# Kernel tuning notes

Hardware: AMD Instinct MI355X
Metric: run time of the kernel (lower is better)

The kernel has to match this reference:

```python
import jax, jax.numpy as jnp
import numpy as np

N, IN_DIM, INTER, HID, OUT, G = 8192, 512, 512, 1024, 512, 16
EPS = 1e-5


def setup_inputs() -> dict:
    key = jax.random.key(0)
    ks = jax.random.split(key, 16)
    s = 0.02
    return {
        "h": jax.random.normal(ks[0], (N, IN_DIM), jnp.float32),
        "D": jax.random.uniform(ks[1], (N, N), jnp.float32),
        "h_prime": jax.random.normal(ks[2], (N, OUT), jnp.float32),
        "Qw": jax.random.normal(ks[3], (IN_DIM, INTER), jnp.float32) * s,
        "Qb": jnp.zeros((INTER,), jnp.float32),
        "Kw": jax.random.normal(ks[4], (IN_DIM, INTER), jnp.float32) * s,
        "Kb": jnp.zeros((INTER,), jnp.float32),
        "Vw": jax.random.normal(ks[5], (IN_DIM, INTER), jnp.float32) * s,
        "Vb": jnp.zeros((INTER,), jnp.float32),
        "Rw": jax.random.normal(ks[6], (INTER, HID), jnp.float32) * s,
        "Rb": jnp.zeros((HID,), jnp.float32),
        "Cw": jax.random.normal(ks[7], (OUT, HID), jnp.float32) * s,
        "Cb": jnp.zeros((HID,), jnp.float32),
        "Pw": jax.random.normal(ks[8], (2 * HID, OUT), jnp.float32) * s,
        "Pb": jnp.zeros((OUT,), jnp.float32),
        "prelu_a": jnp.full((OUT,), 0.25, jnp.float32),  # PReLU default init
        "gn_w": jnp.ones((OUT,), jnp.float32),
        "gn_b": jnp.zeros((OUT,), jnp.float32),
    }


def reference(h, D, h_prime, Qw, Qb, Kw, Kb, Vw, Vb, Rw, Rb, Cw, Cb, Pw, Pb, prelu_a, gn_w, gn_b):
    Q = h @ Qw + Qb                      # (N, inter)
    K = h @ Kw + Kb
    V = h @ Vw + Vb
    scores = D * (Q @ K.T)               # (N, N), decayed retention scores
    h_ret = scores @ V                   # (N, inter)
    h_ret = jax.nn.gelu(h_ret @ Rw + Rb, approximate=False)   # (N, hid)
    h_cat = h_prime @ Cw + Cb            # (N, hid)
    combined = jnp.concatenate([h_ret, h_cat], axis=-1)       # (N, 2*hid)
    x = combined @ Pw + Pb               # (N, out)
    x = jnp.where(x >= 0, x, prelu_a * x)                      # PReLU per-channel
    # GroupNorm over channel groups per row: (N, G, out/G)
    xg = x.reshape(N, G, OUT // G)
    mu = xg.mean(axis=-1, keepdims=True)
    var = xg.var(axis=-1, keepdims=True)
    xn = ((xg - mu) * jax.lax.rsqrt(var + EPS)).reshape(N, OUT)
    return xn * gn_w + gn_b
```

## Files before the change

### kernel.cpp

```cpp
#include <hip/hip_runtime.h>
#include <math.h>

typedef __attribute__((ext_vector_type(8))) short bf16x8;
typedef __attribute__((ext_vector_type(4))) float f32x4;
typedef __attribute__((ext_vector_type(8))) unsigned short u16x8;

#define DEVFN __device__ __forceinline__

DEVFN unsigned short f2bf(float f) {
    unsigned int u = __float_as_uint(f);
    u += 0x7fffu + ((u >> 16) & 1u);
    return (unsigned short)(u >> 16);
}

__global__ void cast2_kernel(const float* __restrict__ a, const float* __restrict__ b,
                             unsigned short* __restrict__ oa, unsigned short* __restrict__ ob,
                             int n8) {
    const float* in = blockIdx.y ? b : a;
    unsigned short* out = blockIdx.y ? ob : oa;
    int i = blockIdx.x * blockDim.x + threadIdx.x;
    if (i >= n8) return;
    const float4* p = reinterpret_cast<const float4*>(in) + (size_t)i * 2;
    float4 x = p[0], y = p[1];
    u16x8 o;
    o[0] = f2bf(x.x); o[1] = f2bf(x.y); o[2] = f2bf(x.z); o[3] = f2bf(x.w);
    o[4] = f2bf(y.x); o[5] = f2bf(y.y); o[6] = f2bf(y.z); o[7] = f2bf(y.w);
    reinterpret_cast<u16x8*>(out)[i] = o;
}

__global__ void sum4_cast_kernel(const float* __restrict__ p, size_t stride,
                                 unsigned short* __restrict__ out, int n8) {
    int i = blockIdx.x * blockDim.x + threadIdx.x;
    if (i >= n8) return;
    const float4* a = reinterpret_cast<const float4*>(p) + (size_t)i * 2;
    const float4* b = reinterpret_cast<const float4*>(p + stride) + (size_t)i * 2;
    const float4* c = reinterpret_cast<const float4*>(p + 2 * stride) + (size_t)i * 2;
    const float4* d = reinterpret_cast<const float4*>(p + 3 * stride) + (size_t)i * 2;
    u16x8 o;
#pragma unroll
    for (int j = 0; j < 2; ++j) {
        float4 va = a[j], vb = b[j], vc = c[j], vd = d[j];
        o[4 * j + 0] = f2bf(va.x + vb.x + vc.x + vd.x);
        o[4 * j + 1] = f2bf(va.y + vb.y + vc.y + vd.y);
        o[4 * j + 2] = f2bf(va.z + vb.z + vc.z + vd.z);
        o[4 * j + 3] = f2bf(va.w + vb.w + vc.w + vd.w);
    }
    reinterpret_cast<u16x8*>(out)[i] = o;
}

__global__ void concat_bias_kernel(const float* __restrict__ a,
                                   const float* __restrict__ b,
                                   const float* __restrict__ c,
                                   float* __restrict__ o) {
    int i = blockIdx.x * blockDim.x + threadIdx.x;
    if (i >= 1536) return;
    o[i] = i < 512 ? a[i] : (i < 1024 ? b[i - 512] : c[i - 1024]);
}

struct TD { const float* in; unsigned short* out; int ldin, ldout, nbx, nby; };
struct TD6 { TD d[6]; };

__global__ void multi_transpose_kernel(TD6 t6) {
    TD d = t6.d[blockIdx.z];
    if ((int)blockIdx.x >= d.nbx || (int)blockIdx.y >= d.nby) return;
    __shared__ unsigned short tile[32][34];
    int c0 = blockIdx.x * 32, r0 = blockIdx.y * 32;
    int tx = threadIdx.x, ty = threadIdx.y;
#pragma unroll
    for (int i = 0; i < 32; i += 8)
        tile[ty + i][tx] = f2bf(d.in[(size_t)(r0 + ty + i) * d.ldin + c0 + tx]);
    __syncthreads();
#pragma unroll
    for (int i = 0; i < 32; i += 8)
        d.out[(size_t)(c0 + ty + i) * d.ldout + r0 + tx] = tile[tx][ty + i];
}

__global__ void transpose_bf16_kernel(const unsigned short* __restrict__ in, int ldin,
                                      unsigned short* __restrict__ out, int ldout) {
    __shared__ unsigned short tile[32][34];
    int c0 = blockIdx.x * 32, r0 = blockIdx.y * 32;
    int tx = threadIdx.x, ty = threadIdx.y;
#pragma unroll
    for (int i = 0; i < 32; i += 8)
        tile[ty + i][tx] = in[(size_t)(r0 + ty + i) * ldin + c0 + tx];
    __syncthreads();
#pragma unroll
    for (int i = 0; i < 32; i += 8)
        out[(size_t)(c0 + ty + i) * ldout + r0 + tx] = tile[tx][ty + i];
}

enum { EP_BF16_BIAS = 0, EP_BF16_DMUL = 1, EP_F32 = 3, EP_PRELU_GN = 4, EP_DUAL = 5 };

template <int MODE>
__global__ __launch_bounds__(256, 2) void gemm_bt_kernel(
    const unsigned short* __restrict__ A, int lda,
    const unsigned short* __restrict__ B, int ldb,
    void* __restrict__ Cv, int ldc, int K,
    const float* __restrict__ bias,
    const float* __restrict__ Dmul, int ldd,
    const float* __restrict__ PA, const float* __restrict__ GW,
    const float* __restrict__ GB, size_t zstride,
    const unsigned short* __restrict__ A2,
    const unsigned short* __restrict__ B2,
    const float* __restrict__ bias2) {
    __shared__ alignas(16) unsigned short As[2][128 * 64];
    __shared__ alignas(16) unsigned short Bs[2][128 * 64];

    unsigned bx, by, zi;
    if (MODE == EP_F32) {
        unsigned gx = gridDim.x;
        unsigned L = (blockIdx.z * gridDim.y + blockIdx.y) * gx + blockIdx.x;
        unsigned xcd = L & 7u, slot = L >> 3;
        zi = xcd >> 1;
        unsigned t = slot * 2 + (xcd & 1u);
        bx = t & (gx - 1);
        by = t / gx;
    } else {
        unsigned nwg = gridDim.x * gridDim.y;
        unsigned bid = blockIdx.y * gridDim.x + blockIdx.x;
        unsigned cpx = nwg >> 3;
        bid = (bid & 7u) * cpx + (bid >> 3);
        bx = bid % gridDim.x;
        by = bid / gridDim.x;
        zi = 0;
    }
    size_t m0 = (size_t)by * 128;
    size_t nB = (size_t)bx * 128;
    size_t ncol0 = nB;

    const unsigned short* Ause = A;
    const unsigned short* Buse = B;
    const float* bias_use = bias;
    bool apply_gelu = false;
    if (MODE == EP_DUAL) {
        unsigned half = gridDim.x >> 1;
        if (bx >= half) {
            nB = (size_t)(bx - half) * 128;
            ncol0 = 1024 + nB;
            Ause = A2; Buse = B2; bias_use = bias2;
        } else {
            apply_gelu = true;
        }
    }

    int tid = threadIdx.x;
    int lane = tid & 63, w = tid >> 6;
    int wr = w >> 1, wc = w & 1;
    int cif = lane & 15;
    int rif = (lane >> 4) << 2;

    f32x4 acc[4][4];
#pragma unroll
    for (int i = 0; i < 4; ++i)
#pragma unroll
        for (int j = 0; j < 4; ++j)
#pragma unroll
            for (int r = 0; r < 4; ++r) acc[i][j][r] = 0.f;

    const unsigned short* Ablk = Ause + m0 * lda + (size_t)zi * K;
    const unsigned short* Bblk = Buse + nB * ldb + (size_t)zi * K;
    int srccol = ((lane & 7) ^ (lane >> 3)) * 8;
    int srow = w * 32 + (lane >> 3);
    int nkt = K >> 6;

    float dreg[4][4][4];

    auto stage = [&](int buf, int kt) {
        int k0 = kt << 6;
        unsigned short* la = &As[buf][w * 2048];
        unsigned short* lb = &Bs[buf][w * 2048];
#pragma unroll
        for (int i = 0; i < 4; ++i) {
            __builtin_amdgcn_global_load_lds(
                (const __attribute__((address_space(1))) void*)(Ablk + (size_t)(srow + i * 8) * lda + k0 + srccol),
                (__attribute__((address_space(3))) void*)(la + i * 512), 16, 0, 0);
            __builtin_amdgcn_global_load_lds(
                (const __attribute__((address_space(1))) void*)(Bblk + (size_t)(srow + i * 8) * ldb + k0 + srccol),
                (__attribute__((address_space(3))) void*)(lb + i * 512), 16, 0, 0);
        }
    };

    stage(0, 0);
    __syncthreads();

    for (int kt = 0; kt < nkt; ++kt) {
        int cur = kt & 1;
        if (kt + 1 < nkt) {
            stage(cur ^ 1, kt + 1);
        } else if (MODE == EP_BF16_DMUL) {
#pragma unroll
            for (int mi = 0; mi < 4; ++mi)
#pragma unroll
                for (int ni = 0; ni < 4; ++ni)
#pragma unroll
                    for (int r = 0; r < 4; ++r)
                        dreg[mi][ni][r] =
                            Dmul[(m0 + wr * 64 + mi * 16 + rif + r) * (size_t)ldd +
                                 (ncol0 + wc * 64 + ni * 16 + cif)];
        }

        const bf16x8* Ap = reinterpret_cast<const bf16x8*>(As[cur]);
        const bf16x8* Bp = reinterpret_cast<const bf16x8*>(Bs[cur]);
#pragma unroll
        for (int kk = 0; kk < 2; ++kk) {
            bf16x8 af[4], bfr[4];
#pragma unroll
            for (int mi = 0; mi < 4; ++mi) {
                int row = wr * 64 + mi * 16 + (lane & 15);
                int slot = ((kk << 2) + (lane >> 4)) ^ (row & 7);
                af[mi] = Ap[row * 8 + slot];
            }
#pragma unroll
            for (int ni = 0; ni < 4; ++ni) {
                int row = wc * 64 + ni * 16 + (lane & 15);
                int slot = ((kk << 2) + (lane >> 4)) ^ (row & 7);
                bfr[ni] = Bp[row * 8 + slot];
            }
#pragma unroll
            for (int mi = 0; mi < 4; ++mi)
#pragma unroll
                for (int ni = 0; ni < 4; ++ni)
                    acc[mi][ni] = __builtin_amdgcn_mfma_f32_16x16x32_bf16(
                        af[mi], bfr[ni], acc[mi][ni], 0, 0, 0);
        }
        __syncthreads();
    }

    if (MODE == EP_PRELU_GN) {
        float* Cf = (float*)Cv;
        float pbv[4], pav[4], gwv[4], gbv[4];
        size_t gcolv[4];
#pragma unroll
        for (int ni = 0; ni < 4; ++ni) {
            gcolv[ni] = ncol0 + wc * 64 + ni * 16 + cif;
            pbv[ni] = bias[gcolv[ni]];
            pav[ni] = PA[gcolv[ni]];
            gwv[ni] = GW[gcolv[ni]];
            gbv[ni] = GB[gcolv[ni]];
        }
#pragma unroll
        for (int mi = 0; mi < 4; ++mi) {
#pragma unroll
            for (int ni = 0; ni < 4; ++ni)
#pragma unroll
                for (int r = 0; r < 4; ++r) {
                    float v = acc[mi][ni][r] + pbv[ni];
                    acc[mi][ni][r] = v >= 0.f ? v : pav[ni] * v;
                }
#pragma unroll
            for (int p = 0; p < 2; ++p) {
                float s[4], ss[4];
#pragma unroll
                for (int r = 0; r < 4; ++r) {
                    float a0 = acc[mi][2 * p][r], a1 = acc[mi][2 * p + 1][r];
                    s[r] = a0 + a1;
                    ss[r] = a0 * a0 + a1 * a1;
                }
#pragma unroll
                for (int msk = 1; msk < 16; msk <<= 1)
#pragma unroll
                    for (int r = 0; r < 4; ++r) {
                        s[r] += __shfl_xor(s[r], msk);
                        ss[r] += __shfl_xor(ss[r], msk);
                    }
#pragma unroll
                for (int r = 0; r < 4; ++r) {
                    float mu = s[r] * (1.f / 32.f);
                    float inv = rsqrtf(ss[r] * (1.f / 32.f) - mu * mu + 1e-5f);
                    size_t grow = m0 + wr * 64 + mi * 16 + rif + r;
#pragma unroll
                    for (int q = 0; q < 2; ++q) {
                        int ni = 2 * p + q;
                        Cf[grow * (size_t)ldc + gcolv[ni]] =
                            (acc[mi][ni][r] - mu) * inv * gwv[ni] + gbv[ni];
                    }
                }
            }
        }
        return;
    }

#pragma unroll
    for (int mi = 0; mi < 4; ++mi) {
#pragma unroll
        for (int ni = 0; ni < 4; ++ni) {
            size_t gcol = ncol0 + wc * 64 + ni * 16 + cif;
            size_t bcol = nB + wc * 64 + ni * 16 + cif;
            float bval = 0.f;
            if (MODE == EP_BF16_BIAS || MODE == EP_DUAL || MODE == EP_F32)
                if (bias_use) bval = bias_use[bcol];
#pragma unroll
            for (int r = 0; r < 4; ++r) {
                size_t grow = m0 + wr * 64 + mi * 16 + rif + r;
                float val = acc[mi][ni][r] + bval;
                if (MODE == EP_BF16_DMUL)
                    val = acc[mi][ni][r] * dreg[mi][ni][r];
                if (MODE == EP_DUAL && apply_gelu)
                    val = 0.5f * val * (1.f + erff(val * 0.70710678118654752f));
                if (MODE == EP_F32) {
                    float* Cf = (float*)Cv + zi * zstride;
                    Cf[grow * (size_t)ldc + gcol] = val;
                } else {
                    ((unsigned short*)Cv)[grow * (size_t)ldc + gcol] = f2bf(val);
                }
            }
        }
    }
}

extern "C" void kernel_launch(void* const* d_in, const int* in_sizes, int n_in,
                              void* d_out, int out_size, void* d_ws, size_t ws_size,
                              hipStream_t stream) {
    constexpr int Nn = 8192, IND = 512, INTER = 512, HID = 1024, OUTD = 512;
    const float* h   = (const float*)d_in[0];
    const float* Dm  = (const float*)d_in[1];
    const float* hp  = (const float*)d_in[2];
    const float* Qw  = (const float*)d_in[3];
    const float* Qb  = (const float*)d_in[4];
    const float* Kw  = (const float*)d_in[5];
    const float* Kb  = (const float*)d_in[6];
    const float* Vw  = (const float*)d_in[7];
    const float* Vb  = (const float*)d_in[8];
    const float* Rw  = (const float*)d_in[9];
    const float* Rb  = (const float*)d_in[10];
    const float* Cw  = (const float*)d_in[11];
    const float* Cb  = (const float*)d_in[12];
    const float* Pw  = (const float*)d_in[13];
    const float* Pb  = (const float*)d_in[14];
    const float* pa  = (const float*)d_in[15];
    const float* gwt = (const float*)d_in[16];
    const float* gbt = (const float*)d_in[17];
    (void)in_sizes; (void)n_in; (void)out_size; (void)ws_size;

    char* ws = (char*)d_ws;
    size_t cur = 0;
    auto alloc = [&](size_t bytes) -> void* {
        void* p = ws + cur;
        cur += (bytes + 255) & ~(size_t)255;
        return p;
    };
    unsigned short* h_bf   = (unsigned short*)alloc((size_t)Nn * IND * 2);
    unsigned short* hp_bf  = (unsigned short*)alloc((size_t)Nn * OUTD * 2);
    unsigned short* QKVwT  = (unsigned short*)alloc((size_t)3 * INTER * IND * 2);
    float*          qkvb   = (float*)alloc((size_t)3 * INTER * 4);
    unsigned short* RwT    = (unsigned short*)alloc((size_t)INTER * HID * 2);
    unsigned short* CwT    = (unsigned short*)alloc((size_t)OUTD * HID * 2);
    unsigned short* PwT    = (unsigned short*)alloc((size_t)2 * HID * OUTD * 2);
    unsigned short* QKVm   = (unsigned short*)alloc((size_t)Nn * 3 * INTER * 2);
    unsigned short* VTm    = (unsigned short*)alloc((size_t)Nn * INTER * 2);
    unsigned short* Sm     = (unsigned short*)alloc((size_t)Nn * Nn * 2);
    float*          hret32 = (float*)alloc((size_t)4 * Nn * INTER * 4);
    unsigned short* hretbf = (unsigned short*)alloc((size_t)Nn * INTER * 2);
    unsigned short* comb   = Sm;

    unsigned short* Qm = QKVm;
    unsigned short* Km = QKVm + INTER;
    unsigned short* Vm = QKVm + 2 * INTER;
    const int ldqkv = 3 * INTER;

    dim3 tb(32, 8);
    int n8 = Nn * IND / 8;
    cast2_kernel<<<dim3(n8 / 256, 2), 256, 0, stream>>>(h, hp, h_bf, hp_bf, n8);

    TD6 t6;
    t6.d[0] = {Qw, QKVwT,                          INTER, IND,     16, 16};
    t6.d[1] = {Kw, QKVwT + (size_t)INTER * IND,    INTER, IND,     16, 16};
    t6.d[2] = {Vw, QKVwT + (size_t)2 * INTER * IND,INTER, IND,     16, 16};
    t6.d[3] = {Rw, RwT,                            HID,   INTER,   32, 16};
    t6.d[4] = {Cw, CwT,                            HID,   OUTD,    32, 16};
    t6.d[5] = {Pw, PwT,                            OUTD,  2 * HID, 16, 64};
    multi_transpose_kernel<<<dim3(32, 64, 6), tb, 0, stream>>>(t6);
    concat_bias_kernel<<<6, 256, 0, stream>>>(Qb, Kb, Vb, qkvb);

    gemm_bt_kernel<EP_BF16_BIAS><<<dim3(3 * INTER / 128, Nn / 128), 256, 0, stream>>>(
        h_bf, IND, QKVwT, IND, QKVm, ldqkv, IND, qkvb, nullptr, 0,
        nullptr, nullptr, nullptr, 0, nullptr, nullptr, nullptr);
    transpose_bf16_kernel<<<dim3(INTER / 32, Nn / 32), tb, 0, stream>>>(Vm, ldqkv, VTm, Nn);

    gemm_bt_kernel<EP_BF16_DMUL><<<dim3(Nn / 128, Nn / 128), 256, 0, stream>>>(
        Qm, ldqkv, Km, ldqkv, Sm, Nn, INTER, nullptr, Dm, Nn,
        nullptr, nullptr, nullptr, 0, nullptr, nullptr, nullptr);

    gemm_bt_kernel<EP_F32><<<dim3(OUTD / 128, Nn / 128, 4), 256, 0, stream>>>(
        Sm, Nn, VTm, Nn, hret32, INTER, Nn / 4, nullptr, nullptr, 0,
        nullptr, nullptr, nullptr, (size_t)Nn * INTER, nullptr, nullptr, nullptr);
    sum4_cast_kernel<<<(Nn * INTER / 8) / 256, 256, 0, stream>>>(
        hret32, (size_t)Nn * INTER, hretbf, Nn * INTER / 8);

    gemm_bt_kernel<EP_DUAL><<<dim3(2 * HID / 128, Nn / 128), 256, 0, stream>>>(
        hretbf, INTER, RwT, INTER, comb, 2 * HID, INTER, Rb, nullptr, 0,
        nullptr, nullptr, nullptr, 0, hp_bf, CwT, Cb);

    gemm_bt_kernel<EP_PRELU_GN><<<dim3(OUTD / 128, Nn / 128), 256, 0, stream>>>(
        comb, 2 * HID, PwT, 2 * HID, d_out, OUTD, 2 * HID, Pb, nullptr, 0,
        pa, gwt, gbt, 0, nullptr, nullptr, nullptr);
}
```

Baseline: 422.6 us.

## Add 256x256 8-wave GEMM with interleaved staging for the two large matmuls

Adds a new GEMM kernel with 256x256 output tiles and 512 threads (8 waves). It interleaves half-tile global-to-LDS loads with four MFMA quadrant phases, using explicit vmcnt waits, barriers and setprio. The kernel handles the QK^T score GEMM (with the D multiply) and the split-K scores@V GEMM. The larger tile raises arithmetic intensity and cuts operand reloads on the dominant N×N work, and the phased schedule overlaps loads with compute. In exchange it uses 128 KB of LDS per block, which may limit occupancy, and the many barriers add sync overhead.

```diff
diff --git a/kernel.cpp b/kernel.cpp
--- a/kernel.cpp
+++ b/kernel.cpp
@@ -6,6 +6,8 @@
 typedef __attribute__((ext_vector_type(8))) unsigned short u16x8;
 
 #define DEVFN __device__ __forceinline__
+#define AS1 __attribute__((address_space(1)))
+#define AS3 __attribute__((address_space(3)))
 
 DEVFN unsigned short f2bf(float f) {
     unsigned int u = __float_as_uint(f);
@@ -89,25 +91,74 @@
         out[(size_t)(c0 + ty + i) * ldout + r0 + tx] = tile[tx][ty + i];
 }
 
-enum { EP_BF16_BIAS = 0, EP_BF16_DMUL = 1, EP_F32 = 3, EP_PRELU_GN = 4, EP_DUAL = 5 };
+enum { P8_DMUL = 0, P8_F32 = 1 };
+
+#define DSREADA(BUF, MH)                                                        \
+    {                                                                           \
+        _Pragma("unroll") for (int q = 0; q < 4; ++q)                           \
+        _Pragma("unroll") for (int kk = 0; kk < 2; ++kk) {                      \
+            int row = ((MH) * 4 + q) * 32 + wm * 16 + (lane & 15);              \
+            int ch = ((kk << 2) + (lane >> 4)) ^ (lane & 7);                    \
+            areg[q][kk] = *(const bf16x8*)&As[BUF][row * 64 + ch * 8];          \
+        }                                                                       \
+    }
+
+#define DSREADB(BUF, NH, BR)                                                    \
+    {                                                                           \
+        _Pragma("unroll") for (int p = 0; p < 2; ++p)                           \
+        _Pragma("unroll") for (int kk = 0; kk < 2; ++kk) {                      \
+            int row = ((NH) * 2 + p) * 64 + wn * 16 + (lane & 15);              \
+            int ch = ((kk << 2) + (lane >> 4)) ^ (lane & 7);                    \
+            BR[p][kk] = *(const bf16x8*)&Bs[BUF][row * 64 + ch * 8];            \
+        }                                                                       \
+    }
+
+#define STAGEA(BUF, HALF, KT)                                                   \
+    {                                                                           \
+        const unsigned short* g0 = Ablk + (size_t)((HALF) * 128 + srow) * lda + (KT) * 64 + src8;       \
+        const unsigned short* g1 = Ablk + (size_t)((HALF) * 128 + 64 + srow) * lda + (KT) * 64 + src8;  \
+        unsigned short* d0 = &As[BUF][(HALF) * 8192 + (w * 64) * 8];            \
+        unsigned short* d1 = &As[BUF][(HALF) * 8192 + (512 + w * 64) * 8];      \
+        __builtin_amdgcn_global_load_lds((const AS1 void*)g0, (AS3 void*)d0, 16, 0, 0); \
+        __builtin_amdgcn_global_load_lds((const AS1 void*)g1, (AS3 void*)d1, 16, 0, 0); \
+    }
+
+#define STAGEB(BUF, HALF, KT)                                                   \
+    {                                                                           \
+        const unsigned short* g0 = Bblk + (size_t)((HALF) * 128 + srow) * ldb + (KT) * 64 + src8;       \
+        const unsigned short* g1 = Bblk + (size_t)((HALF) * 128 + 64 + srow) * ldb + (KT) * 64 + src8;  \
+        unsigned short* d0 = &Bs[BUF][(HALF) * 8192 + (w * 64) * 8];            \
+        unsigned short* d1 = &Bs[BUF][(HALF) * 8192 + (512 + w * 64) * 8];      \
+        __builtin_amdgcn_global_load_lds((const AS1 void*)g0, (AS3 void*)d0, 16, 0, 0); \
+        __builtin_amdgcn_global_load_lds((const AS1 void*)g1, (AS3 void*)d1, 16, 0, 0); \
+    }
+
+#define MMAC(BR, MB, NB)                                                        \
+    {                                                                           \
+        __builtin_amdgcn_s_setprio(1);                                          \
+        _Pragma("unroll") for (int q = 0; q < 4; ++q)                           \
+        _Pragma("unroll") for (int p = 0; p < 2; ++p)                           \
+        _Pragma("unroll") for (int kk = 0; kk < 2; ++kk)                        \
+            acc[(MB) + q][(NB) + p] = __builtin_amdgcn_mfma_f32_16x16x32_bf16(  \
+                areg[q][kk], BR[p][kk], acc[(MB) + q][(NB) + p], 0, 0, 0);      \
+        __builtin_amdgcn_s_setprio(0);                                          \
+    }
+
+#define VMCNT6 asm volatile("s_waitcnt vmcnt(6)" ::: "memory")
+#define VMCNT0 asm volatile("s_waitcnt vmcnt(0)" ::: "memory")
+#define BAR __builtin_amdgcn_s_barrier()
 
 template <int MODE>
-__global__ __launch_bounds__(256, 2) void gemm_bt_kernel(
+__global__ __launch_bounds__(512, 2) void gemm8p_kernel(
     const unsigned short* __restrict__ A, int lda,
     const unsigned short* __restrict__ B, int ldb,
     void* __restrict__ Cv, int ldc, int K,
-    const float* __restrict__ bias,
-    const float* __restrict__ Dmul, int ldd,
-    const float* __restrict__ PA, const float* __restrict__ GW,
-    const float* __restrict__ GB, size_t zstride,
-    const unsigned short* __restrict__ A2,
-    const unsigned short* __restrict__ B2,
-    const float* __restrict__ bias2) {
-    __shared__ alignas(16) unsigned short As[2][128 * 64];
-    __shared__ alignas(16) unsigned short Bs[2][128 * 64];
-
-    unsigned bx, by, zi;
-    if (MODE == EP_F32) {
+    const float* __restrict__ Dmul, int ldd, size_t zstride) {
+    __shared__ alignas(16) unsigned short As[2][256 * 64];
+    __shared__ alignas(16) unsigned short Bs[2][256 * 64];
+
+    unsigned bx, by, zi = 0;
+    if (MODE == P8_F32) {
         unsigned gx = gridDim.x;
         unsigned L = (blockIdx.z * gridDim.y + blockIdx.y) * gx + blockIdx.x;
         unsigned xcd = L & 7u, slot = L >> 3;
@@ -122,8 +173,100 @@
         bid = (bid & 7u) * cpx + (bid >> 3);
         bx = bid % gridDim.x;
         by = bid / gridDim.x;
-        zi = 0;
-    }
+    }
+    size_t m0 = (size_t)by * 256, n0 = (size_t)bx * 256;
+
+    int tid = threadIdx.x;
+    int lane = tid & 63, w = tid >> 6;
+    int wm = w >> 2, wn = w & 3;
+
+    const unsigned short* Ablk = A + m0 * lda + (size_t)zi * K;
+    const unsigned short* Bblk = B + n0 * ldb + (size_t)zi * K;
+    int src8 = ((lane & 7) ^ (lane >> 3)) * 8;
+    int srow = w * 8 + (lane >> 3);
+
+    f32x4 acc[8][4];
+#pragma unroll
+    for (int i = 0; i < 8; ++i)
+#pragma unroll
+        for (int j = 0; j < 4; ++j)
+#pragma unroll
+            for (int r = 0; r < 4; ++r) acc[i][j][r] = 0.f;
+
+    const int NT = K >> 6;
+
+    STAGEA(0, 0, 0); STAGEB(0, 0, 0); STAGEB(0, 1, 0); STAGEA(0, 1, 0);
+    if (NT > 1) { STAGEA(1, 0, 1); STAGEB(1, 0, 1); STAGEB(1, 1, 1); }
+    if (NT > 1) { VMCNT6; } else { VMCNT0; }
+    BAR;
+
+    bf16x8 areg[4][2], breg0[2][2], breg1[2][2];
+
+    for (int t = 0; t < NT; ++t) {
+        int buf = t & 1;
+        DSREADA(buf, 0);
+        DSREADB(buf, 0, breg0);
+        if (t + 1 < NT) STAGEA(buf ^ 1, 1, t + 1);
+        BAR;
+        MMAC(breg0, 0, 0);
+        BAR;
+        DSREADB(buf, 1, breg1);
+        if (t + 2 < NT) STAGEA(buf, 0, t + 2);
+        BAR;
+        MMAC(breg1, 0, 2);
+        BAR;
+        DSREADA(buf, 1);
+        if (t + 2 < NT) STAGEB(buf, 0, t + 2);
+        BAR;
+        MMAC(breg1, 4, 2);
+        BAR;
+        if (t + 2 < NT) { STAGEB(buf, 1, t + 2); VMCNT6; } else { VMCNT0; }
+        BAR;
+        MMAC(breg0, 4, 0);
+        BAR;
+    }
+
+#pragma unroll
+    for (int mi = 0; mi < 8; ++mi) {
+#pragma unroll
+        for (int ni = 0; ni < 4; ++ni) {
+            size_t gcol = n0 + ni * 64 + wn * 16 + (lane & 15);
+#pragma unroll
+            for (int r = 0; r < 4; ++r) {
+                size_t grow = m0 + mi * 32 + wm * 16 + ((lane >> 4) << 2) + r;
+                if (MODE == P8_DMUL) {
+                    float v = acc[mi][ni][r] * Dmul[grow * (size_t)ldd + gcol];
+                    ((unsigned short*)Cv)[grow * (size_t)ldc + gcol] = f2bf(v);
+                } else {
+                    float* Cf = (float*)Cv + zi * zstride;
+                    Cf[grow * (size_t)ldc + gcol] = acc[mi][ni][r];
+                }
+            }
+        }
+    }
+}
+
+enum { EP_BF16_BIAS = 0, EP_PRELU_GN = 4, EP_DUAL = 5 };
+
+template <int MODE>
+__global__ __launch_bounds__(256, 2) void gemm_bt_kernel(
+    const unsigned short* __restrict__ A, int lda,
+    const unsigned short* __restrict__ B, int ldb,
+    void* __restrict__ Cv, int ldc, int K,
+    const float* __restrict__ bias,
+    const float* __restrict__ PA, const float* __restrict__ GW,
+    const float* __restrict__ GB,
+    const unsigned short* __restrict__ A2,
+    const unsigned short* __restrict__ B2,
+    const float* __restrict__ bias2) {
+    __shared__ alignas(16) unsigned short As[2][128 * 64];
+    __shared__ alignas(16) unsigned short Bs[2][128 * 64];
+
+    unsigned nwg = gridDim.x * gridDim.y;
+    unsigned bid = blockIdx.y * gridDim.x + blockIdx.x;
+    unsigned cpx = nwg >> 3;
+    bid = (bid & 7u) * cpx + (bid >> 3);
+    unsigned bx = bid % gridDim.x, by = bid / gridDim.x;
     size_t m0 = (size_t)by * 128;
     size_t nB = (size_t)bx * 128;
     size_t ncol0 = nB;
@@ -157,13 +300,11 @@
 #pragma unroll
             for (int r = 0; r < 4; ++r) acc[i][j][r] = 0.f;
 
-    const unsigned short* Ablk = Ause + m0 * lda + (size_t)zi * K;
-    const unsigned short* Bblk = Buse + nB * ldb + (size_t)zi * K;
+    const unsigned short* Ablk = Ause + m0 * lda;
+    const unsigned short* Bblk = Buse + nB * ldb;
     int srccol = ((lane & 7) ^ (lane >> 3)) * 8;
     int srow = w * 32 + (lane >> 3);
     int nkt = K >> 6;
-
-    float dreg[4][4][4];
 
     auto stage = [&](int buf, int kt) {
         int k0 = kt << 6;
@@ -172,11 +313,11 @@
 #pragma unroll
         for (int i = 0; i < 4; ++i) {
             __builtin_amdgcn_global_load_lds(
-                (const __attribute__((address_space(1))) void*)(Ablk + (size_t)(srow + i * 8) * lda + k0 + srccol),
-                (__attribute__((address_space(3))) void*)(la + i * 512), 16, 0, 0);
+                (const AS1 void*)(Ablk + (size_t)(srow + i * 8) * lda + k0 + srccol),
+                (AS3 void*)(la + i * 512), 16, 0, 0);
             __builtin_amdgcn_global_load_lds(
-                (const __attribute__((address_space(1))) void*)(Bblk + (size_t)(srow + i * 8) * ldb + k0 + srccol),
-                (__attribute__((address_space(3))) void*)(lb + i * 512), 16, 0, 0);
+                (const AS1 void*)(Bblk + (size_t)(srow + i * 8) * ldb + k0 + srccol),
+                (AS3 void*)(lb + i * 512), 16, 0, 0);
         }
     };
 
@@ -185,19 +326,7 @@
 
     for (int kt = 0; kt < nkt; ++kt) {
         int cur = kt & 1;
-        if (kt + 1 < nkt) {
-            stage(cur ^ 1, kt + 1);
-        } else if (MODE == EP_BF16_DMUL) {
-#pragma unroll
-            for (int mi = 0; mi < 4; ++mi)
-#pragma unroll
-                for (int ni = 0; ni < 4; ++ni)
-#pragma unroll
-                    for (int r = 0; r < 4; ++r)
-                        dreg[mi][ni][r] =
-                            Dmul[(m0 + wr * 64 + mi * 16 + rif + r) * (size_t)ldd +
-                                 (ncol0 + wc * 64 + ni * 16 + cif)];
-        }
+        if (kt + 1 < nkt) stage(cur ^ 1, kt + 1);
 
         const bf16x8* Ap = reinterpret_cast<const bf16x8*>(As[cur]);
         const bf16x8* Bp = reinterpret_cast<const bf16x8*>(Bs[cur]);
@@ -286,23 +415,14 @@
         for (int ni = 0; ni < 4; ++ni) {
             size_t gcol = ncol0 + wc * 64 + ni * 16 + cif;
             size_t bcol = nB + wc * 64 + ni * 16 + cif;
-            float bval = 0.f;
-            if (MODE == EP_BF16_BIAS || MODE == EP_DUAL || MODE == EP_F32)
-                if (bias_use) bval = bias_use[bcol];
+            float bval = bias_use ? bias_use[bcol] : 0.f;
 #pragma unroll
             for (int r = 0; r < 4; ++r) {
                 size_t grow = m0 + wr * 64 + mi * 16 + rif + r;
                 float val = acc[mi][ni][r] + bval;
-                if (MODE == EP_BF16_DMUL)
-                    val = acc[mi][ni][r] * dreg[mi][ni][r];
                 if (MODE == EP_DUAL && apply_gelu)
                     val = 0.5f * val * (1.f + erff(val * 0.70710678118654752f));
-                if (MODE == EP_F32) {
-                    float* Cf = (float*)Cv + zi * zstride;
-                    Cf[grow * (size_t)ldc + gcol] = val;
-                } else {
-                    ((unsigned short*)Cv)[grow * (size_t)ldc + gcol] = f2bf(val);
-                }
+                ((unsigned short*)Cv)[grow * (size_t)ldc + gcol] = f2bf(val);
             }
         }
     }
@@ -373,25 +493,23 @@
     concat_bias_kernel<<<6, 256, 0, stream>>>(Qb, Kb, Vb, qkvb);
 
     gemm_bt_kernel<EP_BF16_BIAS><<<dim3(3 * INTER / 128, Nn / 128), 256, 0, stream>>>(
-        h_bf, IND, QKVwT, IND, QKVm, ldqkv, IND, qkvb, nullptr, 0,
-        nullptr, nullptr, nullptr, 0, nullptr, nullptr, nullptr);
+        h_bf, IND, QKVwT, IND, QKVm, ldqkv, IND, qkvb,
+        nullptr, nullptr, nullptr, nullptr, nullptr, nullptr);
     transpose_bf16_kernel<<<dim3(INTER / 32, Nn / 32), tb, 0, stream>>>(Vm, ldqkv, VTm, Nn);
 
-    gemm_bt_kernel<EP_BF16_DMUL><<<dim3(Nn / 128, Nn / 128), 256, 0, stream>>>(
-        Qm, ldqkv, Km, ldqkv, Sm, Nn, INTER, nullptr, Dm, Nn,
-        nullptr, nullptr, nullptr, 0, nullptr, nullptr, nullptr);
-
-    gemm_bt_kernel<EP_F32><<<dim3(OUTD / 128, Nn / 128, 4), 256, 0, stream>>>(
-        Sm, Nn, VTm, Nn, hret32, INTER, Nn / 4, nullptr, nullptr, 0,
-        nullptr, nullptr, nullptr, (size_t)Nn * INTER, nullptr, nullptr, nullptr);
+    gemm8p_kernel<P8_DMUL><<<dim3(Nn / 256, Nn / 256), 512, 0, stream>>>(
+        Qm, ldqkv, Km, ldqkv, Sm, Nn, INTER, Dm, Nn, 0);
+
+    gemm8p_kernel<P8_F32><<<dim3(OUTD / 256, Nn / 256, 4), 512, 0, stream>>>(
+        Sm, Nn, VTm, Nn, hret32, INTER, Nn / 4, nullptr, 0, (size_t)Nn * INTER);
     sum4_cast_kernel<<<(Nn * INTER / 8) / 256, 256, 0, stream>>>(
         hret32, (size_t)Nn * INTER, hretbf, Nn * INTER / 8);
 
     gemm_bt_kernel<EP_DUAL><<<dim3(2 * HID / 128, Nn / 128), 256, 0, stream>>>(
-        hretbf, INTER, RwT, INTER, comb, 2 * HID, INTER, Rb, nullptr, 0,
-        nullptr, nullptr, nullptr, 0, hp_bf, CwT, Cb);
+        hretbf, INTER, RwT, INTER, comb, 2 * HID, INTER, Rb,
+        nullptr, nullptr, nullptr, hp_bf, CwT, Cb);
 
     gemm_bt_kernel<EP_PRELU_GN><<<dim3(OUTD / 128, Nn / 128), 256, 0, stream>>>(
-        comb, 2 * HID, PwT, 2 * HID, d_out, OUTD, 2 * HID, Pb, nullptr, 0,
-        pa, gwt, gbt, 0, nullptr, nullptr, nullptr);
-}
+        comb, 2 * HID, PwT, 2 * HID, d_out, OUTD, 2 * HID, Pb,
+        pa, gwt, gbt, nullptr, nullptr, nullptr);
+}
```

After: 393.2 us. -7.0%, faster.
